# Optimization experiments

Measured on AMD Instinct MI355X. Metric: run time of the kernel, lower is better.

## Reference

```python
import jax, jax.numpy as jnp
import numpy as np

TWO_PI = 2.0 * np.pi
DAMP_VERTICAL = 1.0
DAMP_HORIZONTAL = 0.0


def _var(p, q, ra, rb, wvno, xka, xkb, dpth):
    # surf96 'var': layer eigenfunction products with evanescent-scaling (exp(-pex-sex))
    ra_s = jnp.where(ra > 0, ra, 1.0)
    rb_s = jnp.where(rb > 0, rb, 1.0)
    # P branch
    sinp_o = jnp.sin(p)
    fac_p = jnp.where(p < 16.0, jnp.exp(-2.0 * p), 0.0)
    cosp_e = (1.0 + fac_p) * 0.5
    sinp_e = (1.0 - fac_p) * 0.5
    lt_a = wvno < xka
    gt_a = wvno > xka
    pex = jnp.where(gt_a, p, 0.0)
    cosp = jnp.where(lt_a, jnp.cos(p), jnp.where(gt_a, cosp_e, 1.0))
    w = jnp.where(lt_a, sinp_o / ra_s, jnp.where(gt_a, sinp_e / ra_s, dpth))
    x = jnp.where(lt_a, -ra * sinp_o, jnp.where(gt_a, ra * sinp_e, 0.0))
    # S branch
    sinq_o = jnp.sin(q)
    fac_q = jnp.where(q < 16.0, jnp.exp(-2.0 * q), 0.0)
    cosq_e = (1.0 + fac_q) * 0.5
    sinq_e = (1.0 - fac_q) * 0.5
    lt_b = wvno < xkb
    gt_b = wvno > xkb
    sex = jnp.where(gt_b, q, 0.0)
    cosq = jnp.where(lt_b, jnp.cos(q), jnp.where(gt_b, cosq_e, 1.0))
    y = jnp.where(lt_b, sinq_o / rb_s, jnp.where(gt_b, sinq_e / rb_s, dpth))
    z = jnp.where(lt_b, -rb * sinq_o, jnp.where(gt_b, rb * sinq_e, 0.0))
    exa = pex + sex
    a0 = jnp.where(exa < 60.0, jnp.exp(-exa), 0.0)
    return (a0, cosp * cosq, cosp * y, cosp * z, cosq * w, cosq * x,
            x * y, x * z, w * y, w * z)


def _dnka(wvno2, gam, gammk, rho, a0, cpcq, cpy, cpz, cqw, cqx, xy, xz, wy, wz):
    # Dunkin's 5x5 compound matrix
    gamm1 = gam - 1.0
    twgm1 = gam + gamm1
    gmgmk = gam * gammk
    gmgm1 = gam * gamm1
    gm1sq = gamm1 * gamm1
    rho2 = rho * rho
    a0pq = a0 - cpcq
    t = -2.0 * wvno2
    c00 = cpcq - 2.0 * gmgm1 * a0pq - gmgmk * xz - wvno2 * gm1sq * wy
    c01 = (wvno2 * cpy - cqx) / rho
    c02 = -(twgm1 * a0pq + gammk * xz + wvno2 * gamm1 * wy) / rho
    c03 = (cpz - wvno2 * cqw) / rho
    c04 = -(2.0 * wvno2 * a0pq + xz + wvno2 * wvno2 * wy) / rho2
    c10 = (gmgmk * cpz - gm1sq * cqw) * rho
    c11 = cpcq
    c12 = gammk * cpz - gamm1 * cqw
    c13 = -wz
    c30 = (gm1sq * cpy - gmgmk * cqx) * rho
    c31 = -xy
    c32 = gamm1 * cpy - gammk * cqx
    c40 = -(2.0 * gmgmk * gm1sq * a0pq + gmgmk * gmgmk * xz + gm1sq * gm1sq * wy) * rho2
    c42 = -(gammk * gamm1 * twgm1 * a0pq + gam * gammk * gammk * xz + gamm1 * gm1sq * wy) * rho
    c20 = t * c42
    c21 = t * c32
    c22 = a0 + 2.0 * (cpcq - c00)
    c23 = t * c12
    c24 = t * c02
    rows = [[c00, c01, c02, c03, c04],
            [c10, c11, c12, c13, c03],
            [c20, c21, c22, c23, c24],
            [c30, c31, c32, c11, c01],
            [c40, c30, c42, c10, c00]]
    return jnp.stack([jnp.stack(r, axis=-1) for r in rows], axis=-2)


def _dltar4(wvno, omega, d, a, b, rho):
    # Rayleigh secular function, Dunkin algorithm, no water layer (llw=-1).
    # wvno/omega: (M, *extra) broadcast-compatible; d,a,b,rho: (M, L)
    extra = wvno.ndim - 1
    L = d.shape[-1]

    def lay(x):  # (M, L) -> (L, M, 1, ..., 1)
        return jnp.moveaxis(x, -1, 0).reshape((L, x.shape[0]) + (1,) * extra)

    dL, aL, bL, rhoL = lay(d), lay(a), lay(b), lay(rho)
    omega = jnp.maximum(omega, 1.0e-4)
    wvno2 = wvno * wvno

    # bottom half-space E vector
    xka = omega / aL[L - 1]
    xkb = omega / bL[L - 1]
    ra = jnp.sqrt(jnp.abs(wvno2 - xka * xka))
    rb = jnp.sqrt(jnp.abs(wvno2 - xkb * xkb))
    t = bL[L - 1] / omega
    gammk = 2.0 * t * t
    gam = gammk * wvno2
    gamm1 = gam - 1.0
    r = rhoL[L - 1]
    e = jnp.stack([r * r * (gamm1 * gamm1 - gam * gammk * ra * rb),
                   -r * ra,
                   r * (gamm1 - gammk * ra * rb),
                   r * rb,
                   wvno2 - ra * rb], axis=-1)

    xs = (dL[L - 2::-1], aL[L - 2::-1], bL[L - 2::-1], rhoL[L - 2::-1])

    def step(e, layer):
        dm, am, bm, rm = layer
        xka = omega / am
        xkb = omega / bm
        t = bm / omega
        gammk = 2.0 * t * t
        gam = gammk * wvno2
        ra = jnp.sqrt(jnp.abs(wvno2 - xka * xka))
        rb = jnp.sqrt(jnp.abs(wvno2 - xkb * xkb))
        p = ra * dm
        q = rb * dm
        vt = _var(p, q, ra, rb, wvno, xka, xkb, dm)
        ca = _dnka(wvno2, gam, gammk, rm, *vt)  # (..., 5, 5)
        ee = jnp.einsum('...j,...ji->...i', e, ca)
        t1 = jnp.max(jnp.abs(ee), axis=-1, keepdims=True)
        t1 = jnp.where(t1 < 1.0e-30, 1.0, t1)  # normc numerical-stability rescale
        return ee / t1, None

    e, _ = jax.lax.scan(step, e, xs)
    return e[..., 0]


def _forward(vlist, tlist, d, b, Clist):
    # Brocher empirical relations (initial_method == 'Brocher')
    a = 0.9409 + 2.0947 * b - 0.8206 * b**2 + 0.2683 * b**3 - 0.0251 * b**4
    rho = 1.6612 * a - 0.4721 * a**2 + 0.0671 * a**3 - 0.0043 * a**4 + 0.000106 * a**5

    omega = TWO_PI / tlist          # (M, P)
    wvno = omega / vlist
    e00 = _dltar4(wvno, omega, d, a, b, rho)  # (M, P)

    # normalization grid (torch.no_grad -> stop_gradient)
    omega_g = omega[:, None, :]                   # (M, 1, P)
    wvno_g = omega_g / Clist[None, :, None]       # (M, NC, P)
    det = jax.lax.stop_gradient(_dltar4(wvno_g, omega_g, d, a, b, rho))  # (M, NC, P)

    rng = jnp.max(det, axis=1) - jnp.min(det, axis=1)  # (M, P)
    e00 = e00 / rng
    e00 = jnp.power(0.1, jnp.abs(e00)) - 1.0           # compress_method == 'exp'
    e00_all = jnp.sum(jnp.abs(e00), axis=1) / e00.shape[-1]  # (M,)

    # vertical / horizontal damping regularization
    M, Lv = b.shape
    ev = jnp.eye(Lv, dtype=b.dtype)
    Lmat_v = 2.0 * ev - jnp.eye(Lv, k=1, dtype=b.dtype) - jnp.eye(Lv, k=-1, dtype=b.dtype)
    Lmat_v = Lmat_v.at[0, 0].set(1.0).at[Lv - 1, Lv - 1].set(1.0)
    eh = jnp.eye(M, dtype=b.dtype)
    Lmat_h = 2.0 * eh - jnp.eye(M, k=1, dtype=b.dtype) - jnp.eye(M, k=-1, dtype=b.dtype)
    Lmat_h = Lmat_h.at[0, 0].set(1.0).at[M - 1, M - 1].set(1.0)
    m_v = DAMP_VERTICAL * jnp.einsum('ij,mj->mi', Lmat_v, b) / Lv
    m_h = DAMP_HORIZONTAL * jnp.einsum('nm,ml->nl', Lmat_h, b) / Lv
    return e00_all + jnp.sum(jnp.abs(m_v), axis=1) + jnp.sum(jnp.abs(m_h), axis=1)


def setup_inputs() -> dict:
    key = jax.random.key(0)
    k1, k2, k3, k4 = jax.random.split(key, 4)
    M, L, P, NC = 64, 32, 100, 400
    tlist = jnp.sort(0.5 + 9.5 * jax.random.uniform(k1, (M, P), dtype=jnp.float32), axis=1)  # periods (s)
    vlist = 1.2 + 2.8 * jax.random.uniform(k2, (M, P), dtype=jnp.float32)                    # phase vel (km/s)
    d = 0.2 + 0.8 * jax.random.uniform(k3, (M, L), dtype=jnp.float32)                        # thickness (km)
    b = jnp.sort(1.5 + 3.0 * jax.random.uniform(k4, (M, L), dtype=jnp.float32), axis=1)      # Vs (km/s)
    Clist = jnp.linspace(1.0, 4.8, NC, dtype=jnp.float32)
    return {"vlist": vlist, "tlist": tlist, "d": d, "b": b, "Clist": Clist}


def reference(vlist, tlist, d, b, Clist):
    return _forward(vlist, tlist, d, b, Clist)
```

## Files before the change

kernel.cpp:

```cpp
#include <hip/hip_runtime.h>
#include <math.h>
#include <float.h>

#define Mdim 64
#define Ldim 32
#define Pdim 100
#define NCdim 400
#define EVALS_PER_P (NCdim + 1)
#define EVALS_PER_WAVE 128
#define WAVES_PER_M 314
#define BLOCKS_PER_M 79
#define NPTS (Mdim * Pdim)
#define TWO_PI_F 6.28318530717958647692f
#define LOG2_10TH (-3.3219280948873623f)

typedef float v2 __attribute__((ext_vector_type(2)));

__device__ __forceinline__ v2 mk2(float a, float b) { v2 r; r.x = a; r.y = b; return r; }
__device__ __forceinline__ v2 sel2(bool cx, bool cy, v2 a, v2 b) {
    return mk2(cx ? a.x : b.x, cy ? a.y : b.y);
}

struct alignas(16) LayerP {
    float dm;
    float inv_a2;
    float inv_b2;
    float b2two;
    float rm;
    float inv_rm;
    float inv_rho2;
    float rho2;
};

__device__ __forceinline__ unsigned ord_encode(float f) {
    unsigned u = __float_as_uint(f);
    return (u & 0x80000000u) ? ~u : (u | 0x80000000u);
}
__device__ __forceinline__ float ord_decode(unsigned u) {
    unsigned v = (u & 0x80000000u) ? (u & 0x7FFFFFFFu) : ~u;
    return __uint_as_float(v);
}

template <bool RENORM>
__device__ __forceinline__ void layer_step(const LayerP& L,
                                           v2 wvno2, v2 wvno4, v2 tneg, v2 om2, v2 invom2,
                                           v2& e0, v2& e1, v2& e2, v2& e3, v2& e4)
{
    const float dm = L.dm;

    const v2 ra2 = wvno2 - om2 * L.inv_a2;
    const v2 rb2 = wvno2 - om2 * L.inv_b2;
    const v2 ra = mk2(__builtin_amdgcn_sqrtf(fabsf(ra2.x)),
                      __builtin_amdgcn_sqrtf(fabsf(ra2.y)));
    const v2 rb = mk2(__builtin_amdgcn_sqrtf(fabsf(rb2.x)),
                      __builtin_amdgcn_sqrtf(fabsf(rb2.y)));
    const v2 pp = ra * dm;
    const v2 qq = rb * dm;
    const v2 gammk = L.b2two * invom2;
    const v2 gam   = gammk * wvno2;

    const v2 sp = mk2(__sinf(pp.x), __sinf(pp.y));
    const v2 cp = mk2(__cosf(pp.x), __cosf(pp.y));
    const v2 sq = mk2(__sinf(qq.x), __sinf(qq.y));
    const v2 cq = mk2(__cosf(qq.x), __cosf(qq.y));
    const v2 e_p = mk2(__expf(-pp.x), __expf(-pp.y));
    const v2 e_q = mk2(__expf(-qq.x), __expf(-qq.y));
    const v2 fac_p = e_p * e_p;
    const v2 fac_q = e_q * e_q;
    const v2 cosp_e  =  0.5f * fac_p + 0.5f;
    const v2 sinp_e  = -0.5f * fac_p + 0.5f;
    const v2 msinp_e =  0.5f * fac_p - 0.5f;
    const v2 cosq_e  =  0.5f * fac_q + 0.5f;
    const v2 sinq_e  = -0.5f * fac_q + 0.5f;
    const v2 msinq_e =  0.5f * fac_q - 0.5f;

    const bool lt_ax = ra2.x < 0.0f, lt_ay = ra2.y < 0.0f;
    const bool lt_bx = rb2.x < 0.0f, lt_by = rb2.y < 0.0f;

    const v2 inv_ra = mk2(__builtin_amdgcn_rcpf(ra.x), __builtin_amdgcn_rcpf(ra.y));
    const v2 inv_rb = mk2(__builtin_amdgcn_rcpf(rb.x), __builtin_amdgcn_rcpf(rb.y));

    const v2 cosp = sel2(lt_ax, lt_ay, cp, cosp_e);
    const v2 w = sel2(lt_ax, lt_ay, sp, sinp_e) * inv_ra;
    const v2 x = -(ra * sel2(lt_ax, lt_ay, sp, msinp_e));
    const v2 cosq = sel2(lt_bx, lt_by, cq, cosq_e);
    const v2 y = sel2(lt_bx, lt_by, sq, sinq_e) * inv_rb;
    const v2 z = -(rb * sel2(lt_bx, lt_by, sq, msinq_e));

    const v2 one = mk2(1.0f, 1.0f);
    const v2 a0 = sel2(lt_ax, lt_ay, one, e_p) * sel2(lt_bx, lt_by, one, e_q);

    const v2 cpcq = cosp * cosq;
    const v2 cpy  = cosp * y;
    const v2 cpz  = cosp * z;
    const v2 cqw  = cosq * w;
    const v2 cqx  = cosq * x;
    const v2 xy   = x * y;
    const v2 xz   = x * z;
    const v2 wy   = w * y;
    const v2 wz   = w * z;

    const v2 gamm1 = gam - 1.0f;
    const v2 twgm1 = gam + gamm1;
    const v2 gmgmk = gam * gammk;
    const v2 gmgm1 = gam * gamm1;
    const v2 gm1sq = gamm1 * gamm1;
    const v2 a0pq  = a0 - cpcq;

    const v2 c00 = cpcq - 2.0f * gmgm1 * a0pq - gmgmk * xz - wvno2 * gm1sq * wy;
    const v2 c01 = (wvno2 * cpy - cqx) * L.inv_rm;
    const v2 c02 = -(twgm1 * a0pq + gammk * xz + wvno2 * gamm1 * wy) * L.inv_rm;
    const v2 c03 = (cpz - wvno2 * cqw) * L.inv_rm;
    const v2 c04 = -(2.0f * wvno2 * a0pq + xz + wvno4 * wy) * L.inv_rho2;
    const v2 c10 = (gmgmk * cpz - gm1sq * cqw) * L.rm;
    const v2 c11 = cpcq;
    const v2 c12 = gammk * cpz - gamm1 * cqw;
    const v2 c13 = -wz;
    const v2 c30 = (gm1sq * cpy - gmgmk * cqx) * L.rm;
    const v2 c31 = -xy;
    const v2 c32 = gamm1 * cpy - gammk * cqx;
    const v2 c40 = -(2.0f * gmgmk * gm1sq * a0pq + gmgmk * gmgmk * xz
                     + gm1sq * gm1sq * wy) * L.rho2;
    const v2 c42 = -(gammk * gamm1 * twgm1 * a0pq + gam * gammk * gammk * xz
                     + gamm1 * gm1sq * wy) * L.rm;
    const v2 c22 = a0 + 2.0f * (cpcq - c00);

    const v2 et2 = tneg * e2;

    const v2 ee0 = e0 * c00 + e1 * c10 + et2 * c42 + e3 * c30 + e4 * c40;
    const v2 ee1 = e0 * c01 + e1 * c11 + et2 * c32 + e3 * c31 + e4 * c30;
    const v2 ee2 = e0 * c02 + e1 * c12 + e2  * c22 + e3 * c32 + e4 * c42;
    const v2 ee3 = e0 * c03 + e1 * c13 + et2 * c12 + e3 * c11 + e4 * c10;
    const v2 ee4 = e0 * c04 + e1 * c03 + et2 * c02 + e3 * c01 + e4 * c00;

    if constexpr (RENORM) {
        float t1x = fmaxf(fmaxf(fabsf(ee0.x), fabsf(ee1.x)), fabsf(ee2.x));
        t1x = fmaxf(t1x, fmaxf(fabsf(ee3.x), fabsf(ee4.x)));
        float t1y = fmaxf(fmaxf(fabsf(ee0.y), fabsf(ee1.y)), fabsf(ee2.y));
        t1y = fmaxf(t1y, fmaxf(fabsf(ee3.y), fabsf(ee4.y)));
        t1x = fmaxf(t1x, 1e-30f);
        t1y = fmaxf(t1y, 1e-30f);
        const v2 inv = mk2(__builtin_amdgcn_rcpf(t1x), __builtin_amdgcn_rcpf(t1y));
        e0 = ee0 * inv;
        e1 = ee1 * inv;
        e2 = ee2 * inv;
        e3 = ee3 * inv;
        e4 = ee4 * inv;
    } else {
        e0 = ee0; e1 = ee1; e2 = ee2; e3 = ee3; e4 = ee4;
    }
}

__device__ __forceinline__ v2 dltar4_pk(v2 wvno2, v2 om2, v2 invom2,
                                        const LayerP* __restrict__ slay)
{
    const v2 wvno4 = wvno2 * wvno2;
    const v2 tneg  = -2.0f * wvno2;

    const LayerP H = slay[Ldim - 1];
    const v2 ra2h = wvno2 - om2 * H.inv_a2;
    const v2 rb2h = wvno2 - om2 * H.inv_b2;
    const v2 ra_h = mk2(__builtin_amdgcn_sqrtf(fabsf(ra2h.x)),
                        __builtin_amdgcn_sqrtf(fabsf(ra2h.y)));
    const v2 rb_h = mk2(__builtin_amdgcn_sqrtf(fabsf(rb2h.x)),
                        __builtin_amdgcn_sqrtf(fabsf(rb2h.y)));
    const v2 gammk_h = H.b2two * invom2;
    const v2 gam_h   = gammk_h * wvno2;
    const v2 gamm1_h = gam_h - 1.0f;
    const v2 rarb_h  = ra_h * rb_h;
    v2 e0 = H.rho2 * (gamm1_h * gamm1_h - gam_h * gammk_h * rarb_h);
    v2 e1 = -H.rm * ra_h;
    v2 e2 = H.rm * (gamm1_h - gammk_h * rarb_h);
    v2 e3 = H.rm * rb_h;
    v2 e4 = wvno2 - rarb_h;

    layer_step<true>(slay[Ldim - 2], wvno2, wvno4, tneg, om2, invom2,
                     e0, e1, e2, e3, e4);
    for (int l = Ldim - 3; l >= 1; l -= 2) {
        layer_step<false>(slay[l],     wvno2, wvno4, tneg, om2, invom2,
                          e0, e1, e2, e3, e4);
        layer_step<true> (slay[l - 1], wvno2, wvno4, tneg, om2, invom2,
                          e0, e1, e2, e3, e4);
    }
    return e0;
}

__global__ void init_ws_kernel(unsigned* __restrict__ mxU, unsigned* __restrict__ mnU)
{
    int i = blockIdx.x * blockDim.x + threadIdx.x;
    if (i < NPTS) {
        mxU[i] = 0u;
        mnU[i] = 0xFFFFFFFFu;
    }
}

__global__ __launch_bounds__(256, 5)
void disp_kernel(const float* __restrict__ vlist, const float* __restrict__ tlist,
                 const float* __restrict__ dth,  const float* __restrict__ bvel,
                 const float* __restrict__ Clist,
                 unsigned* __restrict__ mxU, unsigned* __restrict__ mnU,
                 float* __restrict__ e00f)
{
    __shared__ LayerP slay[Ldim];

    const int bid = blockIdx.x;
    const int m   = bid / BLOCKS_PER_M;
    const int wb  = bid - m * BLOCKS_PER_M;
    const int tid  = threadIdx.x;
    const int wid  = tid >> 6;
    const int lane = tid & 63;
    const int wv   = wb * 4 + wid;

    if (tid < Ldim) {
        const float bb = bvel[m * Ldim + tid];
        const float b2 = bb * bb;
        const float b3 = b2 * bb;
        const float b4 = b2 * b2;
        const float aa = 0.9409f + 2.0947f * bb - 0.8206f * b2
                         + 0.2683f * b3 - 0.0251f * b4;
        const float a2 = aa * aa;
        const float a3 = a2 * aa;
        const float a4 = a2 * a2;
        const float a5 = a4 * aa;
        const float rr = 1.6612f * aa - 0.4721f * a2 + 0.0671f * a3
                         - 0.0043f * a4 + 0.000106f * a5;
        LayerP Lp;
        Lp.dm       = dth[m * Ldim + tid];
        Lp.inv_a2   = 1.0f / (aa * aa);
        Lp.inv_b2   = 1.0f / (bb * bb);
        Lp.b2two    = 2.0f * bb * bb;
        Lp.rm       = rr;
        Lp.inv_rm   = 1.0f / rr;
        Lp.inv_rho2 = 1.0f / (rr * rr);
        Lp.rho2     = rr * rr;
        slay[tid] = Lp;
    }
    __syncthreads();

    if (wv >= WAVES_PER_M) return;

    const int S  = wv * EVALS_PER_WAVE;
    const int p0 = S / EVALS_PER_P;
    const int c0 = S - p0 * EVALS_PER_P;

    int cx = c0 + lane;
    const bool crx = cx >= EVALS_PER_P;
    const int px = p0 + (crx ? 1 : 0);
    cx = crx ? cx - EVALS_PER_P : cx;
    const bool validx = px < Pdim;

    int cy = c0 + 64 + lane;
    const bool cry = cy >= EVALS_PER_P;
    const int py = p0 + (cry ? 1 : 0);
    cy = cry ? cy - EVALS_PER_P : cy;
    const bool validy = py < Pdim;

    const int mpx = m * Pdim + (validx ? px : 0);
    const int mpy = m * Pdim + (validy ? py : 0);
    const float omx = fmaxf(TWO_PI_F / tlist[mpx], 1.0e-4f);
    const float omy = fmaxf(TWO_PI_F / tlist[mpy], 1.0e-4f);
    const bool isCx = cx < NCdim;
    const bool isCy = cy < NCdim;
    const float denx = isCx ? Clist[cx] : vlist[mpx];
    const float deny = isCy ? Clist[cy] : vlist[mpy];
    const float wvx = omx / denx;
    const float wvy = omy / deny;

    const v2 om2    = mk2(omx * omx, omy * omy);
    const v2 invom2 = mk2(__builtin_amdgcn_rcpf(om2.x), __builtin_amdgcn_rcpf(om2.y));
    const v2 wvno2  = mk2(wvx * wvx, wvy * wvy);

    const v2 det = dltar4_pk(wvno2, om2, invom2, slay);

    if (validx && !isCx) e00f[m * Pdim + px] = det.x;
    if (validy && !isCy) e00f[m * Pdim + py] = det.y;

    const int pA = p0;
    const int pB = p0 + ((c0 + EVALS_PER_WAVE - 1) >= EVALS_PER_P ? 1 : 0);

    {
        const bool inAx = validx && isCx && (px == pA);
        const bool inAy = validy && isCy && (py == pA);
        float mxA = fmaxf(inAx ? det.x : -FLT_MAX, inAy ? det.y : -FLT_MAX);
        float mnA = fminf(inAx ? det.x :  FLT_MAX, inAy ? det.y :  FLT_MAX);
        for (int off = 32; off >= 1; off >>= 1) {
            mxA = fmaxf(mxA, __shfl_xor(mxA, off));
            mnA = fminf(mnA, __shfl_xor(mnA, off));
        }
        if (lane == 0 && pA < Pdim) {
            atomicMax(&mxU[m * Pdim + pA], ord_encode(mxA));
            atomicMin(&mnU[m * Pdim + pA], ord_encode(mnA));
        }
    }
    if (pB != pA) {
        const bool inBx = validx && isCx && (px == pB);
        const bool inBy = validy && isCy && (py == pB);
        float mxB = fmaxf(inBx ? det.x : -FLT_MAX, inBy ? det.y : -FLT_MAX);
        float mnB = fminf(inBx ? det.x :  FLT_MAX, inBy ? det.y :  FLT_MAX);
        for (int off = 32; off >= 1; off >>= 1) {
            mxB = fmaxf(mxB, __shfl_xor(mxB, off));
            mnB = fminf(mnB, __shfl_xor(mnB, off));
        }
        if (lane == 0 && pB < Pdim) {
            atomicMax(&mxU[m * Pdim + pB], ord_encode(mxB));
            atomicMin(&mnU[m * Pdim + pB], ord_encode(mnB));
        }
    }
}

__global__ __launch_bounds__(64)
void epilogue_kernel(const unsigned* __restrict__ mxU, const unsigned* __restrict__ mnU,
                     const float* __restrict__ e00f, const float* __restrict__ bvel,
                     float* __restrict__ out)
{
    const int m    = blockIdx.x;
    const int lane = threadIdx.x;

    float acc = 0.0f;
    for (int p = lane; p < Pdim; p += 64) {
        const int i = m * Pdim + p;
        const float mx = ord_decode(mxU[i]);
        const float mn = ord_decode(mnU[i]);
        const float en = e00f[i] / (mx - mn);
        acc += 1.0f - __builtin_amdgcn_exp2f(fabsf(en) * LOG2_10TH);
    }

    float damp = 0.0f;
    if (lane < Ldim) {
        const float bb    = bvel[m * Ldim + lane];
        const float bprev = bvel[m * Ldim + ((lane == 0) ? 0 : lane - 1)];
        const float bnext = bvel[m * Ldim + ((lane == Ldim - 1) ? Ldim - 1 : lane + 1)];
        float tval;
        if (lane == 0)             tval = bb - bnext;
        else if (lane == Ldim - 1) tval = bb - bprev;
        else                       tval = 2.0f * bb - bprev - bnext;
        damp = fabsf(tval * (1.0f / (float)Ldim));
    }

    float tot = fmaf(acc, 1.0f / (float)Pdim, damp);
    for (int off = 32; off >= 1; off >>= 1)
        tot += __shfl_xor(tot, off);
    if (lane == 0) out[m] = tot;
}

extern "C" void kernel_launch(void* const* d_in, const int* in_sizes, int n_in,
                              void* d_out, int out_size, void* d_ws, size_t ws_size,
                              hipStream_t stream)
{
    const float* vlist = (const float*)d_in[0];
    const float* tlist = (const float*)d_in[1];
    const float* dth   = (const float*)d_in[2];
    const float* bvel  = (const float*)d_in[3];
    const float* Clist = (const float*)d_in[4];
    float* out = (float*)d_out;

    unsigned* mxU = (unsigned*)d_ws;
    unsigned* mnU = mxU + NPTS;
    float*    e00f = (float*)(mnU + NPTS);

    hipLaunchKernelGGL(init_ws_kernel, dim3((NPTS + 255) / 256), dim3(256), 0, stream,
                       mxU, mnU);
    hipLaunchKernelGGL(disp_kernel, dim3(Mdim * BLOCKS_PER_M), dim3(256), 0, stream,
                       vlist, tlist, dth, bvel, Clist, mxU, mnU, e00f);
    hipLaunchKernelGGL(epilogue_kernel, dim3(Mdim), dim3(64), 0, stream,
                       mxU, mnU, e00f, bvel, out);
}
```

Baseline: 267.2 us.

## Use rsq/hardware trig intrinsics, derive products algebraically, fuse epilogue via last-wave counter

Replaces sqrt+rcp with one rsq per radical and switches to hardware sin/cos/exp2 with pre-scaled arguments, so the wrapped range-reduction code is skipped. Products involving x and z are rewritten as ra2/rb2 times existing w/y products, which saves multiplies and removes the negated-sinh selects. The separate epilogue kernel is removed: each wave bumps a per-model counter, and the last wave to arrive computes the final reduction, saving one kernel launch. Hardware sin/cos take revolutions and lose accuracy for large arguments, and the fence-plus-atomic path adds a small cost to every wave.

After: 394.9 us. +47.8%, slower.

```diff
diff --git a/kernel.cpp b/kernel.cpp
--- a/kernel.cpp
+++ b/kernel.cpp
@@ -12,6 +12,8 @@
 #define BLOCKS_PER_M 79
 #define NPTS (Mdim * Pdim)
 #define TWO_PI_F 6.28318530717958647692f
+#define INV_2PI_F 0.15915494309189535f
+#define NLOG2E_F (-1.4426950408889634f)
 #define LOG2_10TH (-3.3219280948873623f)
 
 typedef float v2 __attribute__((ext_vector_type(2)));
@@ -50,55 +52,55 @@
 
     const v2 ra2 = wvno2 - om2 * L.inv_a2;
     const v2 rb2 = wvno2 - om2 * L.inv_b2;
-    const v2 ra = mk2(__builtin_amdgcn_sqrtf(fabsf(ra2.x)),
-                      __builtin_amdgcn_sqrtf(fabsf(ra2.y)));
-    const v2 rb = mk2(__builtin_amdgcn_sqrtf(fabsf(rb2.x)),
-                      __builtin_amdgcn_sqrtf(fabsf(rb2.y)));
+
+    const v2 inv_ra = mk2(__builtin_amdgcn_rsqf(fabsf(ra2.x)),
+                          __builtin_amdgcn_rsqf(fabsf(ra2.y)));
+    const v2 inv_rb = mk2(__builtin_amdgcn_rsqf(fabsf(rb2.x)),
+                          __builtin_amdgcn_rsqf(fabsf(rb2.y)));
+    const v2 ra = mk2(fabsf(ra2.x), fabsf(ra2.y)) * inv_ra;
+    const v2 rb = mk2(fabsf(rb2.x), fabsf(rb2.y)) * inv_rb;
     const v2 pp = ra * dm;
     const v2 qq = rb * dm;
     const v2 gammk = L.b2two * invom2;
     const v2 gam   = gammk * wvno2;
 
-    const v2 sp = mk2(__sinf(pp.x), __sinf(pp.y));
-    const v2 cp = mk2(__cosf(pp.x), __cosf(pp.y));
-    const v2 sq = mk2(__sinf(qq.x), __sinf(qq.y));
-    const v2 cq = mk2(__cosf(qq.x), __cosf(qq.y));
-    const v2 e_p = mk2(__expf(-pp.x), __expf(-pp.y));
-    const v2 e_q = mk2(__expf(-qq.x), __expf(-qq.y));
+    const v2 ppr = pp * INV_2PI_F;
+    const v2 qqr = qq * INV_2PI_F;
+    const v2 sp = mk2(__builtin_amdgcn_sinf(ppr.x), __builtin_amdgcn_sinf(ppr.y));
+    const v2 cp = mk2(__builtin_amdgcn_cosf(ppr.x), __builtin_amdgcn_cosf(ppr.y));
+    const v2 sq = mk2(__builtin_amdgcn_sinf(qqr.x), __builtin_amdgcn_sinf(qqr.y));
+    const v2 cq = mk2(__builtin_amdgcn_cosf(qqr.x), __builtin_amdgcn_cosf(qqr.y));
+    const v2 pe = pp * NLOG2E_F;
+    const v2 qe = qq * NLOG2E_F;
+    const v2 e_p = mk2(__builtin_amdgcn_exp2f(pe.x), __builtin_amdgcn_exp2f(pe.y));
+    const v2 e_q = mk2(__builtin_amdgcn_exp2f(qe.x), __builtin_amdgcn_exp2f(qe.y));
+
     const v2 fac_p = e_p * e_p;
     const v2 fac_q = e_q * e_q;
-    const v2 cosp_e  =  0.5f * fac_p + 0.5f;
-    const v2 sinp_e  = -0.5f * fac_p + 0.5f;
-    const v2 msinp_e =  0.5f * fac_p - 0.5f;
-    const v2 cosq_e  =  0.5f * fac_q + 0.5f;
-    const v2 sinq_e  = -0.5f * fac_q + 0.5f;
-    const v2 msinq_e =  0.5f * fac_q - 0.5f;
+    const v2 cosp_e = 0.5f * fac_p + 0.5f;
+    const v2 sinp_e = -0.5f * fac_p + 0.5f;
+    const v2 cosq_e = 0.5f * fac_q + 0.5f;
+    const v2 sinq_e = -0.5f * fac_q + 0.5f;
 
     const bool lt_ax = ra2.x < 0.0f, lt_ay = ra2.y < 0.0f;
     const bool lt_bx = rb2.x < 0.0f, lt_by = rb2.y < 0.0f;
 
-    const v2 inv_ra = mk2(__builtin_amdgcn_rcpf(ra.x), __builtin_amdgcn_rcpf(ra.y));
-    const v2 inv_rb = mk2(__builtin_amdgcn_rcpf(rb.x), __builtin_amdgcn_rcpf(rb.y));
-
+    const v2 one = mk2(1.0f, 1.0f);
     const v2 cosp = sel2(lt_ax, lt_ay, cp, cosp_e);
     const v2 w = sel2(lt_ax, lt_ay, sp, sinp_e) * inv_ra;
-    const v2 x = -(ra * sel2(lt_ax, lt_ay, sp, msinp_e));
     const v2 cosq = sel2(lt_bx, lt_by, cq, cosq_e);
     const v2 y = sel2(lt_bx, lt_by, sq, sinq_e) * inv_rb;
-    const v2 z = -(rb * sel2(lt_bx, lt_by, sq, msinq_e));
-
-    const v2 one = mk2(1.0f, 1.0f);
     const v2 a0 = sel2(lt_ax, lt_ay, one, e_p) * sel2(lt_bx, lt_by, one, e_q);
 
     const v2 cpcq = cosp * cosq;
     const v2 cpy  = cosp * y;
-    const v2 cpz  = cosp * z;
     const v2 cqw  = cosq * w;
-    const v2 cqx  = cosq * x;
-    const v2 xy   = x * y;
-    const v2 xz   = x * z;
     const v2 wy   = w * y;
-    const v2 wz   = w * z;
+    const v2 cpz  = rb2 * cpy;
+    const v2 cqx  = ra2 * cqw;
+    const v2 wz   = rb2 * wy;
+    const v2 xy   = ra2 * wy;
+    const v2 xz   = ra2 * wz;
 
     const v2 gamm1 = gam - 1.0f;
     const v2 twgm1 = gam + gamm1;
@@ -185,13 +187,15 @@
     return e0;
 }
 
-__global__ void init_ws_kernel(unsigned* __restrict__ mxU, unsigned* __restrict__ mnU)
+__global__ void init_ws_kernel(unsigned* __restrict__ mxU, unsigned* __restrict__ mnU,
+                               unsigned* __restrict__ cnt)
 {
     int i = blockIdx.x * blockDim.x + threadIdx.x;
     if (i < NPTS) {
         mxU[i] = 0u;
         mnU[i] = 0xFFFFFFFFu;
     }
+    if (i < Mdim) cnt[i] = 0u;
 }
 
 __global__ __launch_bounds__(256, 5)
@@ -199,7 +203,8 @@
                  const float* __restrict__ dth,  const float* __restrict__ bvel,
                  const float* __restrict__ Clist,
                  unsigned* __restrict__ mxU, unsigned* __restrict__ mnU,
-                 float* __restrict__ e00f)
+                 float* __restrict__ e00f, unsigned* __restrict__ cnt,
+                 float* __restrict__ out)
 {
     __shared__ LayerP slay[Ldim];
 
@@ -306,41 +311,45 @@
             atomicMin(&mnU[m * Pdim + pB], ord_encode(mnB));
         }
     }
-}
-
-__global__ __launch_bounds__(64)
-void epilogue_kernel(const unsigned* __restrict__ mxU, const unsigned* __restrict__ mnU,
-                     const float* __restrict__ e00f, const float* __restrict__ bvel,
-                     float* __restrict__ out)
-{
-    const int m    = blockIdx.x;
-    const int lane = threadIdx.x;
-
-    float acc = 0.0f;
-    for (int p = lane; p < Pdim; p += 64) {
-        const int i = m * Pdim + p;
-        const float mx = ord_decode(mxU[i]);
-        const float mn = ord_decode(mnU[i]);
-        const float en = e00f[i] / (mx - mn);
-        acc += 1.0f - __builtin_amdgcn_exp2f(fabsf(en) * LOG2_10TH);
-    }
-
-    float damp = 0.0f;
-    if (lane < Ldim) {
-        const float bb    = bvel[m * Ldim + lane];
-        const float bprev = bvel[m * Ldim + ((lane == 0) ? 0 : lane - 1)];
-        const float bnext = bvel[m * Ldim + ((lane == Ldim - 1) ? Ldim - 1 : lane + 1)];
-        float tval;
-        if (lane == 0)             tval = bb - bnext;
-        else if (lane == Ldim - 1) tval = bb - bprev;
-        else                       tval = 2.0f * bb - bprev - bnext;
-        damp = fabsf(tval * (1.0f / (float)Ldim));
-    }
-
-    float tot = fmaf(acc, 1.0f / (float)Pdim, damp);
-    for (int off = 32; off >= 1; off >>= 1)
-        tot += __shfl_xor(tot, off);
-    if (lane == 0) out[m] = tot;
+
+    __threadfence();
+    unsigned old = 0u;
+    if (lane == 0) old = atomicAdd(&cnt[m], 1u);
+    const int last = __shfl((lane == 0 && old == WAVES_PER_M - 1) ? 1 : 0, 0);
+    if (last) {
+        __threadfence();
+
+        float acc = 0.0f;
+        for (int p = lane; p < Pdim; p += 64) {
+            const int i = m * Pdim + p;
+            const unsigned umx = __hip_atomic_load(&mxU[i], __ATOMIC_RELAXED,
+                                                   __HIP_MEMORY_SCOPE_AGENT);
+            const unsigned umn = __hip_atomic_load(&mnU[i], __ATOMIC_RELAXED,
+                                                   __HIP_MEMORY_SCOPE_AGENT);
+            const float e00v = __hip_atomic_load(&e00f[i], __ATOMIC_RELAXED,
+                                                 __HIP_MEMORY_SCOPE_AGENT);
+            const float rng = ord_decode(umx) - ord_decode(umn);
+            const float en  = e00v / rng;
+            acc += 1.0f - __builtin_amdgcn_exp2f(fabsf(en) * LOG2_10TH);
+        }
+
+        float damp = 0.0f;
+        if (lane < Ldim) {
+            const float bb    = bvel[m * Ldim + lane];
+            const float bprev = bvel[m * Ldim + ((lane == 0) ? 0 : lane - 1)];
+            const float bnext = bvel[m * Ldim + ((lane == Ldim - 1) ? Ldim - 1 : lane + 1)];
+            float tval;
+            if (lane == 0)             tval = bb - bnext;
+            else if (lane == Ldim - 1) tval = bb - bprev;
+            else                       tval = 2.0f * bb - bprev - bnext;
+            damp = fabsf(tval * (1.0f / (float)Ldim));
+        }
+
+        float tot = fmaf(acc, 1.0f / (float)Pdim, damp);
+        for (int off = 32; off >= 1; off >>= 1)
+            tot += __shfl_xor(tot, off);
+        if (lane == 0) out[m] = tot;
+    }
 }
 
 extern "C" void kernel_launch(void* const* d_in, const int* in_sizes, int n_in,
@@ -357,11 +366,10 @@
     unsigned* mxU = (unsigned*)d_ws;
     unsigned* mnU = mxU + NPTS;
     float*    e00f = (float*)(mnU + NPTS);
+    unsigned* cnt  = (unsigned*)(e00f + NPTS);
 
     hipLaunchKernelGGL(init_ws_kernel, dim3((NPTS + 255) / 256), dim3(256), 0, stream,
-                       mxU, mnU);
+                       mxU, mnU, cnt);
     hipLaunchKernelGGL(disp_kernel, dim3(Mdim * BLOCKS_PER_M), dim3(256), 0, stream,
-                       vlist, tlist, dth, bvel, Clist, mxU, mnU, e00f);
-    hipLaunchKernelGGL(epilogue_kernel, dim3(Mdim), dim3(64), 0, stream,
-                       mxU, mnU, e00f, bvel, out);
-}
+                       vlist, tlist, dth, bvel, Clist, mxU, mnU, e00f, cnt, out);
+}
```
